# Kernel optimization log

Hardware: AMD Instinct MI355X
Metric: run time of the kernel (lower is better)

Reference implementation:

```python
import jax, jax.numpy as jnp
import numpy as np

GROUP_SIZE = 128
EPS = 1e-6
# AWQ nibble interleave order within each int32
_AWQ_SHIFTS = jnp.array([0, 4, 1, 5, 2, 6, 3, 7], dtype=jnp.uint32) * 4


def dequant_awq(qw, qz, sc, group_size=GROUP_SIZE):
    # qw: (in, out//8) int32, qz: (in//g, out//8) int32, sc: (in//g, out) float
    in_dim = qw.shape[0]
    w4 = ((qw.astype(jnp.uint32)[:, :, None] >> _AWQ_SHIFTS) & 0xF).astype(sc.dtype)
    z4 = ((qz.astype(jnp.uint32)[:, :, None] >> _AWQ_SHIFTS) & 0xF).astype(sc.dtype)
    w4 = w4.reshape(in_dim, -1)                    # (in, out)
    z4 = z4.reshape(qz.shape[0], -1)               # (in//g, out)
    z = jnp.repeat(z4, group_size, axis=0)         # (in, out)
    s = jnp.repeat(sc, group_size, axis=0)         # (in, out)
    return (w4 - z) * s


def rmsnorm(x, w, eps=EPS):
    return x * w * jax.lax.rsqrt(jnp.mean(x * x, axis=-1, keepdims=True) + eps)


def setup_inputs() -> dict:
    key = jax.random.key(0)
    ks = jax.random.split(key, 16)
    H, I, G = 2048, 8192, GROUP_SIZE
    IMAX = 2**31 - 1
    d = {}
    d['x'] = jax.random.normal(ks[0], (2, 2048, H), dtype=jnp.float32)
    d['ln1_w'] = jnp.ones((H,), jnp.float32)
    d['ln2_w'] = jnp.ones((H,), jnp.float32)
    d['qkv_qw'] = jax.random.randint(ks[1], (H, 3 * H // 8), 0, IMAX, dtype=jnp.int32)
    d['qkv_qz'] = jax.random.randint(ks[2], (H // G, 3 * H // 8), 0, IMAX, dtype=jnp.int32)
    d['qkv_sc'] = jax.random.normal(ks[3], (H // G, 3 * H), dtype=jnp.float32) * 0.02
    d['o_qw'] = jax.random.randint(ks[4], (H, H // 8), 0, IMAX, dtype=jnp.int32)
    d['o_qz'] = jax.random.randint(ks[5], (H // G, H // 8), 0, IMAX, dtype=jnp.int32)
    d['o_sc'] = jax.random.normal(ks[6], (H // G, H), dtype=jnp.float32) * 0.02
    d['gu_qw'] = jax.random.randint(ks[7], (H, 2 * I // 8), 0, IMAX, dtype=jnp.int32)
    d['gu_qz'] = jax.random.randint(ks[8], (H // G, 2 * I // 8), 0, IMAX, dtype=jnp.int32)
    d['gu_sc'] = jax.random.normal(ks[9], (H // G, 2 * I), dtype=jnp.float32) * 0.02
    d['dn_qw'] = jax.random.randint(ks[10], (I, H // 8), 0, IMAX, dtype=jnp.int32)
    d['dn_qz'] = jax.random.randint(ks[11], (I // G, H // 8), 0, IMAX, dtype=jnp.int32)
    d['dn_sc'] = jax.random.normal(ks[12], (I // G, H), dtype=jnp.float32) * 0.02
    return d


def reference(x, ln1_w, ln2_w, qkv_qw, qkv_qz, qkv_sc, o_qw, o_qz, o_sc,
              gu_qw, gu_qz, gu_sc, dn_qw, dn_qz, dn_sc):
    H = x.shape[-1]
    # attention-ish block (mock: qkv proj, take q slice, o proj)
    residual = x
    h = rmsnorm(x, ln1_w)
    qkv = h @ dequant_awq(qkv_qw, qkv_qz, qkv_sc)          # (..., 3H)
    q = qkv[..., :H]
    o = q @ dequant_awq(o_qw, o_qz, o_sc)                  # (..., H)
    x = residual + o
    # SwiGLU MLP
    residual = x
    h = rmsnorm(x, ln2_w)
    gate_up = h @ dequant_awq(gu_qw, gu_qz, gu_sc)         # (..., 2I)
    gate, up = jnp.split(gate_up, 2, axis=-1)
    mlp = (jax.nn.silu(gate) * up) @ dequant_awq(dn_qw, dn_qz, dn_sc)
    return residual + mlp
```

## Files before the change

kernel.cpp:

```cpp
#include <hip/hip_runtime.h>
#include <hip/hip_bf16.h>
#include <stdint.h>

typedef __bf16 bf16x8 __attribute__((ext_vector_type(8)));
typedef __bf16 bf16x2 __attribute__((ext_vector_type(2)));
typedef float  f32x4  __attribute__((ext_vector_type(4)));

template <int V> struct ic { static constexpr int value = V; };

__device__ __forceinline__ void gload_lds16(const void* g, void* l) {
  __builtin_amdgcn_global_load_lds(
      (const __attribute__((address_space(1))) void*)g,
      (__attribute__((address_space(3))) void*)l, 16, 0, 0);
}

__global__ __launch_bounds__(256) void rmsnorm_kernel(
    const float* __restrict__ x, const float* __restrict__ w,
    __bf16* __restrict__ out) {
  constexpr int H = 2048;
  const int row = blockIdx.x;
  const int t = threadIdx.x;
  const float4* xr = (const float4*)(x + (size_t)row * H);
  float4 a = xr[t * 2 + 0];
  float4 b = xr[t * 2 + 1];
  float ss = a.x*a.x + a.y*a.y + a.z*a.z + a.w*a.w
           + b.x*b.x + b.y*b.y + b.z*b.z + b.w*b.w;
#pragma unroll
  for (int o = 32; o > 0; o >>= 1) ss += __shfl_xor(ss, o);
  __shared__ float red[4];
  if ((t & 63) == 0) red[t >> 6] = ss;
  __syncthreads();
  float tot = red[0] + red[1] + red[2] + red[3];
  float r = rsqrtf(tot * (1.0f / H) + 1e-6f);
  const float4* wr4 = (const float4*)w;
  float4 wa = wr4[t * 2 + 0];
  float4 wb = wr4[t * 2 + 1];
  bf16x8 ov;
  ov[0] = (__bf16)(a.x * wa.x * r);
  ov[1] = (__bf16)(a.y * wa.y * r);
  ov[2] = (__bf16)(a.z * wa.z * r);
  ov[3] = (__bf16)(a.w * wa.w * r);
  ov[4] = (__bf16)(b.x * wb.x * r);
  ov[5] = (__bf16)(b.y * wb.y * r);
  ov[6] = (__bf16)(b.z * wb.z * r);
  ov[7] = (__bf16)(b.w * wb.w * r);
  *(bf16x8*)(out + (size_t)row * H + (size_t)t * 8) = ov;
}

template <int GU>
__global__ __launch_bounds__(256) void dequant_t_kernel(
    const int* __restrict__ qw, const int* __restrict__ qz,
    const float* __restrict__ sc, __bf16* __restrict__ wt,
    int K, int Cp, int Nfull) {
  const int t = threadIdx.x;
  const int k0 = blockIdx.x * 128 + (t & 63) * 2;
  const int c0 = blockIdx.y * 64 + (t >> 6) * 16;
  const int g = k0 >> 7;
  const uint32_t* qw0 = (const uint32_t*)qw + (size_t)k0 * Cp + c0;
  const uint32_t* qw1 = qw0 + Cp;
  const uint32_t* qzr = (const uint32_t*)qz + (size_t)g * Cp + c0;
  const float* scr = sc + (size_t)g * Nfull + (size_t)c0 * 8;

  uint32_t u0[16], u1[16], z[16];
#pragma unroll
  for (int j = 0; j < 4; j++) {
    *(int4*)(&u0[j*4]) = *(const int4*)(qw0 + j*4);
    *(int4*)(&u1[j*4]) = *(const int4*)(qw1 + j*4);
    *(int4*)(&z[j*4])  = *(const int4*)(qzr + j*4);
  }

#pragma unroll
  for (int i = 0; i < 16; i++) {
#pragma unroll
    for (int s = 0; s < 8; s++) {
      const int sh = ((s >> 1) * 4) + ((s & 1) ? 16 : 0);
      const float zf = (float)((z[i] >> sh) & 15u);
      const float scv = scr[i * 8 + s];
      const float w0 = ((float)((u0[i] >> sh) & 15u) - zf) * scv;
      const float w1 = ((float)((u1[i] >> sh) & 15u) - zf) * scv;
      const int n = (c0 + i) * 8 + s;
      int row;
      if (GU) row = (n < 8192) ? ((n >> 4) * 32 + (n & 15))
                               : (((n - 8192) >> 4) * 32 + 16 + (n & 15));
      else    row = n;
      bf16x2 pv = {(__bf16)w0, (__bf16)w1};
      *(bf16x2*)(wt + (size_t)row * K + k0) = pv;
    }
  }
}

template <int BN, int EPI, int KC>
__global__ __launch_bounds__(512, 2) void gemm8p_kernel(
    const __bf16* __restrict__ A, const __bf16* __restrict__ Bt,
    void* __restrict__ Cv, const float* __restrict__ addend,
    int M, int N) {
  constexpr int NT = KC / 64;
  constexpr int BQ = BN / 64;
  constexpr int NSTRIP = BN / 4;
  constexpr int NI = NSTRIP / 16;

  __shared__ alignas(16) __bf16 As[8 * 4096];
  __shared__ alignas(16) __bf16 Bs[2 * BQ * 4096];

  const int t = threadIdx.x;
  const int w = t >> 6, l = t & 63;
  const int lm = l & 15, kb = l >> 4;
  const int l7 = lm & 7;
  const int wm = w >> 2, wn = w & 3;

  const size_t stat = (size_t)(t >> 3) * KC + (size_t)(((t & 7) ^ ((t >> 3) & 7)) << 3);

  const int nwg = gridDim.x;
  const int bid = blockIdx.x;
  const int swz = (bid & 7) * (nwg >> 3) + (bid >> 3);
  const int nbm = M >> 8;
  const int per_g = nbm * 8;
  const int grp = swz / per_g, v = swz % per_g;
  const int bm0 = (v % nbm) * 256;
  const int bn0 = (grp * 8 + v / nbm) * BN;

  const __bf16* Ab = A + (size_t)bm0 * KC;
  const __bf16* Bb = Bt + (size_t)bn0 * KC;

  const uint32_t gsw0 = (uint32_t)((kb ^ l7) << 4);
  const uint32_t gsw1 = (uint32_t)(((4 + kb) ^ l7) << 4);
  const uint32_t arow = (uint32_t)(wm * 16384 + lm * 128);
  const uint32_t aoff0 = arow + gsw0, aoff1 = arow + gsw1;
  const uint32_t brow = (BN == 256)
      ? (uint32_t)(wn * 8192 + lm * 128)
      : (uint32_t)((wn >> 1) * 8192 + (wn & 1) * 4096 + lm * 128);
  const uint32_t boff0 = brow + gsw0, boff1 = brow + gsw1;
  const char* AsC = (const char*)As;
  const char* BsC = (const char*)Bs;

  f32x4 acc[8][NI] = {};
  bf16x8 af[2][2][2];
  bf16x8 bfr[2][NI][2];

  auto ldAf = [&](int dD, int mi, bf16x8* dst) {
    const uint32_t imA = (uint32_t)((dD * 4 + (mi >> 2)) * 8192 + (mi & 3) * 2048);
    dst[0] = *(const bf16x8*)(AsC + aoff0 + imA);
    dst[1] = *(const bf16x8*)(AsC + aoff1 + imA);
  };
  auto ldBf = [&](int dD) {
#pragma unroll
    for (int ni = 0; ni < NI; ++ni) {
      const uint32_t imB = (uint32_t)(dD * BQ * 8192 + ni * 2048);
      bfr[dD][ni][0] = *(const bf16x8*)(BsC + boff0 + imB);
      bfr[dD][ni][1] = *(const bf16x8*)(BsC + boff1 + imB);
    }
  };
  auto mfma4 = [&](int q, bf16x8 afq[2][2], int dD) {
    __builtin_amdgcn_s_setprio(1);
#pragma unroll
    for (int kk = 0; kk < 2; ++kk)
#pragma unroll
      for (int ni = 0; ni < NI; ++ni)
#pragma unroll
        for (int m2 = 0; m2 < 2; ++m2)
          acc[q * 2 + m2][ni] = __builtin_amdgcn_mfma_f32_16x16x32_bf16(
              afq[m2][kk], bfr[dD][ni][kk], acc[q * 2 + m2][ni], 0, 0, 0);
    __builtin_amdgcn_s_setprio(0);
  };

#pragma unroll
  for (int qa = 0; qa < 4; ++qa)
    gload_lds16(Ab + stat + (size_t)(qa * 64) * KC, As + qa * 4096 + t * 8);
#pragma unroll
  for (int qb = 0; qb < BQ; ++qb)
    gload_lds16(Bb + stat + (size_t)(qb * 64) * KC, Bs + qb * 4096 + t * 8);
#pragma unroll
  for (int qb = 0; qb < BQ; ++qb)
    gload_lds16(Bb + stat + (size_t)(qb * 64) * KC + 64, Bs + (BQ + qb) * 4096 + t * 8);
  gload_lds16(Ab + stat + 64, As + 4 * 4096 + t * 8);
  gload_lds16(Ab + stat + (size_t)128 * KC + 64, As + 6 * 4096 + t * 8);
  if (BN == 256) asm volatile("s_waitcnt vmcnt(6)" ::: "memory");
  else           asm volatile("s_waitcnt vmcnt(4)" ::: "memory");
  __builtin_amdgcn_s_barrier();

  ldAf(0, 0, af[0][0]); ldAf(0, 1, af[0][1]);
  ldBf(0);
  asm volatile("" ::: "memory");

  const __bf16* pA0 = Ab + stat + 128;
  const __bf16* pA1 = Ab + stat + (size_t)64 * KC + 64;
  const __bf16* pA2 = Ab + stat + (size_t)128 * KC + 128;
  const __bf16* pA3 = Ab + stat + (size_t)192 * KC + 64;
  const __bf16* pB0 = Bb + stat + 128;
  const __bf16* pB1 = Bb + stat + (size_t)64 * KC + 128;
  const __bf16* pB2 = Bb + stat + (size_t)128 * KC + 128;
  const __bf16* pB3 = Bb + stat + (size_t)192 * KC + 128;

  auto tile = [&](auto Dc, auto Sc) {
    constexpr int D = decltype(Dc)::value;
    constexpr int STG = decltype(Sc)::value;
    ldAf(D, 2, af[1][0]); ldAf(D, 3, af[1][1]);
    asm volatile("" ::: "memory");
    if (STG >= 1) {
      gload_lds16(pA1, As + ((D ^ 1) * 4 + 1) * 4096 + t * 8);
      gload_lds16(pA3, As + ((D ^ 1) * 4 + 3) * 4096 + t * 8);
    }
    __builtin_amdgcn_s_barrier();
    mfma4(0, af[0], D);
    __builtin_amdgcn_s_barrier();
    ldAf(D, 4, af[0][0]); ldAf(D, 5, af[0][1]);
    asm volatile("" ::: "memory");
    if (STG == 2) {
      gload_lds16(pB0, Bs + (D * BQ + 0) * 4096 + t * 8);
      gload_lds16(pB1, Bs + (D * BQ + 1) * 4096 + t * 8);
    }
    __builtin_amdgcn_s_barrier();
    mfma4(1, af[1], D);
    __builtin_amdgcn_s_barrier();
    ldAf(D, 6, af[1][0]); ldAf(D, 7, af[1][1]);
    asm volatile("" ::: "memory");
    if (STG == 2) {
      if (BN == 256) {
        gload_lds16(pB2, Bs + (D * BQ + 2) * 4096 + t * 8);
        gload_lds16(pB3, Bs + (D * BQ + 3) * 4096 + t * 8);
      } else {
        gload_lds16(pA0, As + (D * 4 + 0) * 4096 + t * 8);
        gload_lds16(pA2, As + (D * 4 + 2) * 4096 + t * 8);
      }
    }
    __builtin_amdgcn_s_barrier();
    mfma4(2, af[0], D);
    __builtin_amdgcn_s_barrier();
    asm volatile("s_waitcnt lgkmcnt(0)" ::: "memory");
    __builtin_amdgcn_sched_barrier(0);
    if (STG == 2)      asm volatile("s_waitcnt vmcnt(4)" ::: "memory");
    else if (STG == 1) asm volatile("s_waitcnt vmcnt(0)" ::: "memory");
    __builtin_amdgcn_s_barrier();
    if (STG >= 1) {
      ldAf(D ^ 1, 0, af[0][0]); ldAf(D ^ 1, 1, af[0][1]);
      ldBf(D ^ 1);
    }
    if (STG == 2 && BN == 256) {
      gload_lds16(pA0, As + (D * 4 + 0) * 4096 + t * 8);
      gload_lds16(pA2, As + (D * 4 + 2) * 4096 + t * 8);
    }
    __builtin_amdgcn_sched_barrier(0);
    mfma4(3, af[1], D);
    __builtin_amdgcn_s_barrier();
    if (STG == 2) {
      pA0 += 64; pA1 += 64; pA2 += 64; pA3 += 64;
      pB0 += 64; pB1 += 64;
      if (BN == 256) { pB2 += 64; pB3 += 64; }
    }
  };

#pragma unroll 1
  for (int it = 0; it < NT / 2 - 1; ++it) {
    tile(ic<0>{}, ic<2>{});
    tile(ic<1>{}, ic<2>{});
  }
  tile(ic<0>{}, ic<1>{});
  tile(ic<1>{}, ic<0>{});

  const int crow0 = bm0 + wm * 128;
#pragma unroll
  for (int mi = 0; mi < 8; ++mi) {
    if (EPI == 2) {
#pragma unroll
      for (int p = 0; p < NI / 2; ++p) {
        const int ni = p * 2;
        const int col = ((bn0 + wn * 64 + ni * 16) >> 5) * 16 + lm;
#pragma unroll
        for (int r = 0; r < 4; ++r) {
          const int row = crow0 + mi * 16 + kb * 4 + r;
          const float gv = acc[mi][ni][r], uv = acc[mi][ni + 1][r];
          const float av = uv * (gv / (1.0f + __expf(-gv)));
          ((__bf16*)Cv)[(size_t)row * 8192 + col] = (__bf16)av;
        }
      }
    } else {
#pragma unroll
      for (int ni = 0; ni < NI; ++ni) {
        const int col = bn0 + wn * NSTRIP + ni * 16 + lm;
#pragma unroll
        for (int r = 0; r < 4; ++r) {
          const int row = crow0 + mi * 16 + kb * 4 + r;
          const size_t idx = (size_t)row * N + col;
          if (EPI == 0) ((__bf16*)Cv)[idx] = (__bf16)acc[mi][ni][r];
          else          ((float*)Cv)[idx] = addend[idx] + acc[mi][ni][r];
        }
      }
    }
  }
}

template <int EPI, int KC>
__global__ __launch_bounds__(512, 4) void gemm128_kernel(
    const __bf16* __restrict__ A, const __bf16* __restrict__ Bt,
    void* __restrict__ Cv, const float* __restrict__ addend,
    int M, int N) {
  constexpr int NT = KC / 64;

  __shared__ alignas(16) __bf16 As[4 * 4096];
  __shared__ alignas(16) __bf16 Bs[4 * 4096];

  const int t = threadIdx.x;
  const int w = t >> 6, l = t & 63;
  const int lm = l & 15, kb = l >> 4;
  const int l7 = lm & 7;
  const int wm = w >> 2, wn = w & 3;

  const size_t stat = (size_t)(t >> 3) * KC + (size_t)(((t & 7) ^ ((t >> 3) & 7)) << 3);

  const int nwg = gridDim.x;
  const int bid = blockIdx.x;
  const int swz = (bid & 7) * (nwg >> 3) + (bid >> 3);
  const int nbm = M >> 7;
  const int per_g = nbm * 8;
  const int grp = swz / per_g, v = swz % per_g;
  const int bm0 = (v % nbm) * 128;
  const int bn0 = (grp * 8 + v / nbm) * 128;

  const __bf16* Ab = A + (size_t)bm0 * KC;
  const __bf16* Bb = Bt + (size_t)bn0 * KC;

  const uint32_t gsw0 = (uint32_t)((kb ^ l7) << 4);
  const uint32_t gsw1 = (uint32_t)(((4 + kb) ^ l7) << 4);
  const uint32_t aoff0 = (uint32_t)((wm * 32 + lm) * 128) + gsw0;
  const uint32_t aoff1 = (uint32_t)((wm * 32 + lm) * 128) + gsw1;
  const uint32_t bbase = (uint32_t)(((wn & 1) * 32 + lm) * 128 + (wn >> 1) * 8192);
  const uint32_t boff0 = bbase + gsw0, boff1 = bbase + gsw1;
  const char* AsC = (const char*)As;
  const char* BsC = (const char*)Bs;

  f32x4 acc[4][2] = {};
  bf16x8 af[2][2];
  bf16x8 bfr[2][2][2];

  auto ldAf = [&](int dD, int mi) {
    const uint32_t imA = (uint32_t)((dD * 2 + (mi >> 1)) * 8192 + (mi & 1) * 2048);
    af[mi & 1][0] = *(const bf16x8*)(AsC + aoff0 + imA);
    af[mi & 1][1] = *(const bf16x8*)(AsC + aoff1 + imA);
  };
  auto ldBf = [&](int dD) {
#pragma unroll
    for (int ni = 0; ni < 2; ++ni) {
      const uint32_t imB = (uint32_t)(dD * 16384 + ni * 2048);
      bfr[dD][ni][0] = *(const bf16x8*)(BsC + boff0 + imB);
      bfr[dD][ni][1] = *(const bf16x8*)(BsC + boff1 + imB);
    }
  };
  auto mfma1 = [&](int mi, int dD) {
    __builtin_amdgcn_s_setprio(1);
#pragma unroll
    for (int kk = 0; kk < 2; ++kk)
#pragma unroll
      for (int ni = 0; ni < 2; ++ni)
        acc[mi][ni] = __builtin_amdgcn_mfma_f32_16x16x32_bf16(
            af[mi & 1][kk], bfr[dD][ni][kk], acc[mi][ni], 0, 0, 0);
    __builtin_amdgcn_s_setprio(0);
  };

  gload_lds16(Ab + stat,                        As + 0 * 4096 + t * 8);
  gload_lds16(Ab + stat + (size_t)64 * KC,      As + 1 * 4096 + t * 8);
  gload_lds16(Bb + stat,                        Bs + 0 * 4096 + t * 8);
  gload_lds16(Bb + stat + (size_t)64 * KC,      Bs + 1 * 4096 + t * 8);
  gload_lds16(Bb + stat + 64,                   Bs + 2 * 4096 + t * 8);
  gload_lds16(Bb + stat + (size_t)64 * KC + 64, Bs + 3 * 4096 + t * 8);
  gload_lds16(Ab + stat + 64,                   As + 2 * 4096 + t * 8);
  asm volatile("s_waitcnt vmcnt(3)" ::: "memory");
  __builtin_amdgcn_s_barrier();

  ldAf(0, 0);
  ldBf(0);
  asm volatile("" ::: "memory");

  const __bf16* pAq1 = Ab + stat + (size_t)64 * KC + 64;
  const __bf16* pAq0 = Ab + stat + 128;
  const __bf16* pBq0 = Bb + stat + 128;
  const __bf16* pBq1 = Bb + stat + (size_t)64 * KC + 128;

  auto tile = [&](auto Dc, auto Sc) {
    constexpr int D = decltype(Dc)::value;
    constexpr int STG = decltype(Sc)::value;
    ldAf(D, 1);
    asm volatile("" ::: "memory");
    if (STG >= 1)
      gload_lds16(pAq1, As + ((D ^ 1) * 2 + 1) * 4096 + t * 8);
    __builtin_amdgcn_s_barrier();
    mfma1(0, D);
    __builtin_amdgcn_s_barrier();
    ldAf(D, 2);
    asm volatile("" ::: "memory");
    if (STG == 2) {
      gload_lds16(pBq0, Bs + (D * 2 + 0) * 4096 + t * 8);
      gload_lds16(pBq1, Bs + (D * 2 + 1) * 4096 + t * 8);
    }
    __builtin_amdgcn_s_barrier();
    mfma1(1, D);
    __builtin_amdgcn_s_barrier();
    ldAf(D, 3);
    asm volatile("" ::: "memory");
    if (STG == 2)
      gload_lds16(pAq0, As + (D * 2 + 0) * 4096 + t * 8);
    __builtin_amdgcn_s_barrier();
    mfma1(2, D);
    __builtin_amdgcn_s_barrier();
    asm volatile("s_waitcnt lgkmcnt(0)" ::: "memory");
    __builtin_amdgcn_sched_barrier(0);
    if (STG == 2)      asm volatile("s_waitcnt vmcnt(3)" ::: "memory");
    else if (STG == 1) asm volatile("s_waitcnt vmcnt(0)" ::: "memory");
    __builtin_amdgcn_s_barrier();
    if (STG >= 1) {
      ldAf(D ^ 1, 0);
      ldBf(D ^ 1);
    }
    __builtin_amdgcn_sched_barrier(0);
    mfma1(3, D);
    __builtin_amdgcn_s_barrier();
    if (STG == 2) { pAq0 += 64; pAq1 += 64; pBq0 += 64; pBq1 += 64; }
  };

#pragma unroll 1
  for (int it = 0; it < NT / 2 - 1; ++it) {
    tile(ic<0>{}, ic<2>{});
    tile(ic<1>{}, ic<2>{});
  }
  tile(ic<0>{}, ic<1>{});
  tile(ic<1>{}, ic<0>{});

#pragma unroll
  for (int mi = 0; mi < 4; ++mi) {
#pragma unroll
    for (int ni = 0; ni < 2; ++ni) {
      const int col = bn0 + wn * 32 + ni * 16 + lm;
#pragma unroll
      for (int r = 0; r < 4; ++r) {
        const int row = bm0 + (mi >> 1) * 64 + wm * 32 + (mi & 1) * 16 + kb * 4 + r;
        const size_t idx = (size_t)row * N + col;
        if (EPI == 0) ((__bf16*)Cv)[idx] = (__bf16)acc[mi][ni][r];
        else          ((float*)Cv)[idx] = addend[idx] + acc[mi][ni][r];
      }
    }
  }
}

extern "C" void kernel_launch(void* const* d_in, const int* in_sizes, int n_in,
                              void* d_out, int out_size, void* d_ws, size_t ws_size,
                              hipStream_t stream) {
  const float* x      = (const float*)d_in[0];
  const float* ln1    = (const float*)d_in[1];
  const float* ln2    = (const float*)d_in[2];
  const int*   qkv_qw = (const int*)d_in[3];
  const int*   qkv_qz = (const int*)d_in[4];
  const float* qkv_sc = (const float*)d_in[5];
  const int*   o_qw   = (const int*)d_in[6];
  const int*   o_qz   = (const int*)d_in[7];
  const float* o_sc   = (const float*)d_in[8];
  const int*   gu_qw  = (const int*)d_in[9];
  const int*   gu_qz  = (const int*)d_in[10];
  const float* gu_sc  = (const float*)d_in[11];
  const int*   dn_qw  = (const int*)d_in[12];
  const int*   dn_qz  = (const int*)d_in[13];
  const float* dn_sc  = (const float*)d_in[14];

  constexpr int M = 4096;

  char* ws = (char*)d_ws;
  __bf16* h   = (__bf16*)(ws + 0);
  __bf16* q   = (__bf16*)(ws + 16777216ULL);
  float*  x2  = (float*)(ws + 33554432ULL);
  __bf16* W   = (__bf16*)(ws + 67108864ULL);
  __bf16* act = (__bf16*)(ws + 134217728ULL);
  __bf16* Wdn = (__bf16*)(ws + 0);

  rmsnorm_kernel<<<dim3(M), dim3(256), 0, stream>>>(x, ln1, h);
  dequant_t_kernel<0><<<dim3(16, 4), dim3(256), 0, stream>>>(qkv_qw, qkv_qz, qkv_sc, W, 2048, 768, 6144);
  gemm128_kernel<0, 2048><<<dim3(512), dim3(512), 0, stream>>>(h, W, (void*)q, nullptr, M, 2048);
  dequant_t_kernel<0><<<dim3(16, 4), dim3(256), 0, stream>>>(o_qw, o_qz, o_sc, W, 2048, 256, 2048);
  gemm128_kernel<1, 2048><<<dim3(512), dim3(512), 0, stream>>>(q, W, (void*)x2, x, M, 2048);
  rmsnorm_kernel<<<dim3(M), dim3(256), 0, stream>>>(x2, ln2, h);
  dequant_t_kernel<1><<<dim3(16, 32), dim3(256), 0, stream>>>(gu_qw, gu_qz, gu_sc, W, 2048, 2048, 16384);
  gemm8p_kernel<256, 2, 2048><<<dim3(1024), dim3(512), 0, stream>>>(h, W, (void*)act, nullptr, M, 16384);
  dequant_t_kernel<0><<<dim3(64, 4), dim3(256), 0, stream>>>(dn_qw, dn_qz, dn_sc, Wdn, 8192, 256, 2048);
  gemm128_kernel<1, 8192><<<dim3(512), dim3(512), 0, stream>>>(act, Wdn, d_out, x2, M, 2048);
}
```

Before: 516.1 us.

## Restructure GEMM inner tiles into quadrant MFMA blocks with in-tile fragment loads

The big gate/up GEMM is specialised to a 256-wide tile, and its inner loop changes from four row-strip MFMA phases into four quadrant phases (4x2 MFMA blocks). Each phase loads its A half and B pair from LDS inside the same tile, which removes the cross-tile prefetch of fragments for the next buffer. The 128 GEMM gets the same quadrant restructure. This cuts register pressure and simplifies the waits. The cost is that LDS fragment loads are no longer hidden behind the previous tile's MFMAs, so phases may stall on LDS latency.

After: 542.3 us. 5.1% more time.

```diff
diff --git a/kernel.cpp b/kernel.cpp
--- a/kernel.cpp
+++ b/kernel.cpp
@@ -89,18 +89,14 @@
   }
 }
 
-template <int BN, int EPI, int KC>
-__global__ __launch_bounds__(512, 2) void gemm8p_kernel(
+template <int KC>
+__global__ __launch_bounds__(512, 2) void gemm256_kernel(
     const __bf16* __restrict__ A, const __bf16* __restrict__ Bt,
-    void* __restrict__ Cv, const float* __restrict__ addend,
-    int M, int N) {
+    __bf16* __restrict__ act, int M) {
   constexpr int NT = KC / 64;
-  constexpr int BQ = BN / 64;
-  constexpr int NSTRIP = BN / 4;
-  constexpr int NI = NSTRIP / 16;
 
   __shared__ alignas(16) __bf16 As[8 * 4096];
-  __shared__ alignas(16) __bf16 Bs[2 * BQ * 4096];
+  __shared__ alignas(16) __bf16 Bs[8 * 4096];
 
   const int t = threadIdx.x;
   const int w = t >> 6, l = t & 63;
@@ -117,7 +113,7 @@
   const int per_g = nbm * 8;
   const int grp = swz / per_g, v = swz % per_g;
   const int bm0 = (v % nbm) * 256;
-  const int bn0 = (grp * 8 + v / nbm) * BN;
+  const int bn0 = (grp * 8 + v / nbm) * 256;
 
   const __bf16* Ab = A + (size_t)bm0 * KC;
   const __bf16* Bb = Bt + (size_t)bn0 * KC;
@@ -126,40 +122,43 @@
   const uint32_t gsw1 = (uint32_t)(((4 + kb) ^ l7) << 4);
   const uint32_t arow = (uint32_t)(wm * 16384 + lm * 128);
   const uint32_t aoff0 = arow + gsw0, aoff1 = arow + gsw1;
-  const uint32_t brow = (BN == 256)
-      ? (uint32_t)(wn * 8192 + lm * 128)
-      : (uint32_t)((wn >> 1) * 8192 + (wn & 1) * 4096 + lm * 128);
+  const uint32_t brow = (uint32_t)(wn * 8192 + lm * 128);
   const uint32_t boff0 = brow + gsw0, boff1 = brow + gsw1;
   const char* AsC = (const char*)As;
   const char* BsC = (const char*)Bs;
 
-  f32x4 acc[8][NI] = {};
-  bf16x8 af[2][2][2];
-  bf16x8 bfr[2][NI][2];
-
-  auto ldAf = [&](int dD, int mi, bf16x8* dst) {
-    const uint32_t imA = (uint32_t)((dD * 4 + (mi >> 2)) * 8192 + (mi & 3) * 2048);
-    dst[0] = *(const bf16x8*)(AsC + aoff0 + imA);
-    dst[1] = *(const bf16x8*)(AsC + aoff1 + imA);
-  };
-  auto ldBf = [&](int dD) {
-#pragma unroll
-    for (int ni = 0; ni < NI; ++ni) {
-      const uint32_t imB = (uint32_t)(dD * BQ * 8192 + ni * 2048);
-      bfr[dD][ni][0] = *(const bf16x8*)(BsC + boff0 + imB);
-      bfr[dD][ni][1] = *(const bf16x8*)(BsC + boff1 + imB);
-    }
-  };
-  auto mfma4 = [&](int q, bf16x8 afq[2][2], int dD) {
+  f32x4 acc[8][4] = {};
+  bf16x8 af4[4][2];
+  bf16x8 bfr4[4][2];
+
+  auto ldAhalf = [&](int dD, int half) {
+#pragma unroll
+    for (int m2 = 0; m2 < 4; ++m2) {
+      const int mi = half * 4 + m2;
+      const uint32_t imA = (uint32_t)((dD * 4 + (mi >> 2)) * 8192 + (mi & 3) * 2048);
+      af4[m2][0] = *(const bf16x8*)(AsC + aoff0 + imA);
+      af4[m2][1] = *(const bf16x8*)(AsC + aoff1 + imA);
+    }
+  };
+  auto ldBpair = [&](int dD, int p) {
+#pragma unroll
+    for (int j = 0; j < 2; ++j) {
+      const int ni = p * 2 + j;
+      const uint32_t imB = (uint32_t)(dD * 32768 + ni * 2048);
+      bfr4[ni][0] = *(const bf16x8*)(BsC + boff0 + imB);
+      bfr4[ni][1] = *(const bf16x8*)(BsC + boff1 + imB);
+    }
+  };
+  auto mfmaQ = [&](int qm, int qn) {
     __builtin_amdgcn_s_setprio(1);
 #pragma unroll
     for (int kk = 0; kk < 2; ++kk)
 #pragma unroll
-      for (int ni = 0; ni < NI; ++ni)
-#pragma unroll
-        for (int m2 = 0; m2 < 2; ++m2)
-          acc[q * 2 + m2][ni] = __builtin_amdgcn_mfma_f32_16x16x32_bf16(
-              afq[m2][kk], bfr[dD][ni][kk], acc[q * 2 + m2][ni], 0, 0, 0);
+      for (int j = 0; j < 2; ++j)
+#pragma unroll
+        for (int m2 = 0; m2 < 4; ++m2)
+          acc[qm * 4 + m2][qn * 2 + j] = __builtin_amdgcn_mfma_f32_16x16x32_bf16(
+              af4[m2][kk], bfr4[qn * 2 + j][kk], acc[qm * 4 + m2][qn * 2 + j], 0, 0, 0);
     __builtin_amdgcn_s_setprio(0);
   };
 
@@ -167,20 +166,15 @@
   for (int qa = 0; qa < 4; ++qa)
     gload_lds16(Ab + stat + (size_t)(qa * 64) * KC, As + qa * 4096 + t * 8);
 #pragma unroll
-  for (int qb = 0; qb < BQ; ++qb)
+  for (int qb = 0; qb < 4; ++qb)
     gload_lds16(Bb + stat + (size_t)(qb * 64) * KC, Bs + qb * 4096 + t * 8);
 #pragma unroll
-  for (int qb = 0; qb < BQ; ++qb)
-    gload_lds16(Bb + stat + (size_t)(qb * 64) * KC + 64, Bs + (BQ + qb) * 4096 + t * 8);
+  for (int qb = 0; qb < 4; ++qb)
+    gload_lds16(Bb + stat + (size_t)(qb * 64) * KC + 64, Bs + (4 + qb) * 4096 + t * 8);
   gload_lds16(Ab + stat + 64, As + 4 * 4096 + t * 8);
   gload_lds16(Ab + stat + (size_t)128 * KC + 64, As + 6 * 4096 + t * 8);
-  if (BN == 256) asm volatile("s_waitcnt vmcnt(6)" ::: "memory");
-  else           asm volatile("s_waitcnt vmcnt(4)" ::: "memory");
+  asm volatile("s_waitcnt vmcnt(6)" ::: "memory");
   __builtin_amdgcn_s_barrier();
-
-  ldAf(0, 0, af[0][0]); ldAf(0, 1, af[0][1]);
-  ldBf(0);
-  asm volatile("" ::: "memory");
 
   const __bf16* pA0 = Ab + stat + 128;
   const __bf16* pA1 = Ab + stat + (size_t)64 * KC + 64;
@@ -194,58 +188,46 @@
   auto tile = [&](auto Dc, auto Sc) {
     constexpr int D = decltype(Dc)::value;
     constexpr int STG = decltype(Sc)::value;
-    ldAf(D, 2, af[1][0]); ldAf(D, 3, af[1][1]);
+    ldAhalf(D, 0);
+    ldBpair(D, 0);
     asm volatile("" ::: "memory");
     if (STG >= 1) {
       gload_lds16(pA1, As + ((D ^ 1) * 4 + 1) * 4096 + t * 8);
       gload_lds16(pA3, As + ((D ^ 1) * 4 + 3) * 4096 + t * 8);
     }
     __builtin_amdgcn_s_barrier();
-    mfma4(0, af[0], D);
-    __builtin_amdgcn_s_barrier();
-    ldAf(D, 4, af[0][0]); ldAf(D, 5, af[0][1]);
+    mfmaQ(0, 0);
+    __builtin_amdgcn_s_barrier();
+    ldBpair(D, 1);
+    asm volatile("" ::: "memory");
+    __builtin_amdgcn_s_barrier();
+    mfmaQ(0, 1);
+    __builtin_amdgcn_s_barrier();
+    ldAhalf(D, 1);
     asm volatile("" ::: "memory");
     if (STG == 2) {
-      gload_lds16(pB0, Bs + (D * BQ + 0) * 4096 + t * 8);
-      gload_lds16(pB1, Bs + (D * BQ + 1) * 4096 + t * 8);
-    }
-    __builtin_amdgcn_s_barrier();
-    mfma4(1, af[1], D);
-    __builtin_amdgcn_s_barrier();
-    ldAf(D, 6, af[1][0]); ldAf(D, 7, af[1][1]);
-    asm volatile("" ::: "memory");
+      gload_lds16(pB0, Bs + (D * 4 + 0) * 4096 + t * 8);
+      gload_lds16(pB1, Bs + (D * 4 + 1) * 4096 + t * 8);
+    }
+    __builtin_amdgcn_s_barrier();
+    mfmaQ(1, 0);
+    __builtin_amdgcn_s_barrier();
+    if (STG == 2)      asm volatile("s_waitcnt vmcnt(2)" ::: "memory");
+    else if (STG == 1) asm volatile("s_waitcnt vmcnt(0)" ::: "memory");
+    __builtin_amdgcn_sched_barrier(0);
+    __builtin_amdgcn_s_barrier();
     if (STG == 2) {
-      if (BN == 256) {
-        gload_lds16(pB2, Bs + (D * BQ + 2) * 4096 + t * 8);
-        gload_lds16(pB3, Bs + (D * BQ + 3) * 4096 + t * 8);
-      } else {
-        gload_lds16(pA0, As + (D * 4 + 0) * 4096 + t * 8);
-        gload_lds16(pA2, As + (D * 4 + 2) * 4096 + t * 8);
-      }
-    }
-    __builtin_amdgcn_s_barrier();
-    mfma4(2, af[0], D);
-    __builtin_amdgcn_s_barrier();
-    asm volatile("s_waitcnt lgkmcnt(0)" ::: "memory");
-    __builtin_amdgcn_sched_barrier(0);
-    if (STG == 2)      asm volatile("s_waitcnt vmcnt(4)" ::: "memory");
-    else if (STG == 1) asm volatile("s_waitcnt vmcnt(0)" ::: "memory");
-    __builtin_amdgcn_s_barrier();
-    if (STG >= 1) {
-      ldAf(D ^ 1, 0, af[0][0]); ldAf(D ^ 1, 1, af[0][1]);
-      ldBf(D ^ 1);
-    }
-    if (STG == 2 && BN == 256) {
+      gload_lds16(pB2, Bs + (D * 4 + 2) * 4096 + t * 8);
+      gload_lds16(pB3, Bs + (D * 4 + 3) * 4096 + t * 8);
       gload_lds16(pA0, As + (D * 4 + 0) * 4096 + t * 8);
       gload_lds16(pA2, As + (D * 4 + 2) * 4096 + t * 8);
     }
     __builtin_amdgcn_sched_barrier(0);
-    mfma4(3, af[1], D);
+    mfmaQ(1, 1);
     __builtin_amdgcn_s_barrier();
     if (STG == 2) {
       pA0 += 64; pA1 += 64; pA2 += 64; pA3 += 64;
-      pB0 += 64; pB1 += 64;
-      if (BN == 256) { pB2 += 64; pB3 += 64; }
+      pB0 += 64; pB1 += 64; pB2 += 64; pB3 += 64;
     }
   };
 
@@ -260,30 +242,16 @@
   const int crow0 = bm0 + wm * 128;
 #pragma unroll
   for (int mi = 0; mi < 8; ++mi) {
-    if (EPI == 2) {
-#pragma unroll
-      for (int p = 0; p < NI / 2; ++p) {
-        const int ni = p * 2;
-        const int col = ((bn0 + wn * 64 + ni * 16) >> 5) * 16 + lm;
-#pragma unroll
-        for (int r = 0; r < 4; ++r) {
-          const int row = crow0 + mi * 16 + kb * 4 + r;
-          const float gv = acc[mi][ni][r], uv = acc[mi][ni + 1][r];
-          const float av = uv * (gv / (1.0f + __expf(-gv)));
-          ((__bf16*)Cv)[(size_t)row * 8192 + col] = (__bf16)av;
-        }
-      }
-    } else {
-#pragma unroll
-      for (int ni = 0; ni < NI; ++ni) {
-        const int col = bn0 + wn * NSTRIP + ni * 16 + lm;
-#pragma unroll
-        for (int r = 0; r < 4; ++r) {
-          const int row = crow0 + mi * 16 + kb * 4 + r;
-          const size_t idx = (size_t)row * N + col;
-          if (EPI == 0) ((__bf16*)Cv)[idx] = (__bf16)acc[mi][ni][r];
-          else          ((float*)Cv)[idx] = addend[idx] + acc[mi][ni][r];
-        }
+#pragma unroll
+    for (int p = 0; p < 2; ++p) {
+      const int ni = p * 2;
+      const int col = ((bn0 + wn * 64 + ni * 16) >> 5) * 16 + lm;
+#pragma unroll
+      for (int r = 0; r < 4; ++r) {
+        const int row = crow0 + mi * 16 + kb * 4 + r;
+        const float gv = acc[mi][ni][r], uv = acc[mi][ni + 1][r];
+        const float av = uv * (gv / (1.0f + __expf(-gv)));
+        act[(size_t)row * 8192 + col] = (__bf16)av;
       }
     }
   }
@@ -329,30 +297,31 @@
   const char* BsC = (const char*)Bs;
 
   f32x4 acc[4][2] = {};
-  bf16x8 af[2][2];
-  bf16x8 bfr[2][2][2];
-
-  auto ldAf = [&](int dD, int mi) {
-    const uint32_t imA = (uint32_t)((dD * 2 + (mi >> 1)) * 8192 + (mi & 1) * 2048);
-    af[mi & 1][0] = *(const bf16x8*)(AsC + aoff0 + imA);
-    af[mi & 1][1] = *(const bf16x8*)(AsC + aoff1 + imA);
-  };
-  auto ldBf = [&](int dD) {
-#pragma unroll
-    for (int ni = 0; ni < 2; ++ni) {
-      const uint32_t imB = (uint32_t)(dD * 16384 + ni * 2048);
-      bfr[dD][ni][0] = *(const bf16x8*)(BsC + boff0 + imB);
-      bfr[dD][ni][1] = *(const bf16x8*)(BsC + boff1 + imB);
-    }
-  };
-  auto mfma1 = [&](int mi, int dD) {
+  bf16x8 af2[2][2];
+  bf16x8 bfrq[2][2];
+
+  auto ldApair = [&](int dD, int half) {
+#pragma unroll
+    for (int m2 = 0; m2 < 2; ++m2) {
+      const int mi = half * 2 + m2;
+      const uint32_t imA = (uint32_t)((dD * 2 + (mi >> 1)) * 8192 + (mi & 1) * 2048);
+      af2[m2][0] = *(const bf16x8*)(AsC + aoff0 + imA);
+      af2[m2][1] = *(const bf16x8*)(AsC + aoff1 + imA);
+    }
+  };
+  auto ldBq = [&](int dD, int ni) {
+    const uint32_t imB = (uint32_t)(dD * 16384 + ni * 2048);
+    bfrq[ni][0] = *(const bf16x8*)(BsC + boff0 + imB);
+    bfrq[ni][1] = *(const bf16x8*)(BsC + boff1 + imB);
+  };
+  auto mfmaQ = [&](int qm, int ni) {
     __builtin_amdgcn_s_setprio(1);
 #pragma unroll
     for (int kk = 0; kk < 2; ++kk)
 #pragma unroll
-      for (int ni = 0; ni < 2; ++ni)
-        acc[mi][ni] = __builtin_amdgcn_mfma_f32_16x16x32_bf16(
-            af[mi & 1][kk], bfr[dD][ni][kk], acc[mi][ni], 0, 0, 0);
+      for (int m2 = 0; m2 < 2; ++m2)
+        acc[qm * 2 + m2][ni] = __builtin_amdgcn_mfma_f32_16x16x32_bf16(
+            af2[m2][kk], bfrq[ni][kk], acc[qm * 2 + m2][ni], 0, 0, 0);
     __builtin_amdgcn_s_setprio(0);
   };
 
@@ -366,10 +335,6 @@
   asm volatile("s_waitcnt vmcnt(3)" ::: "memory");
   __builtin_amdgcn_s_barrier();
 
-  ldAf(0, 0);
-  ldBf(0);
-  asm volatile("" ::: "memory");
-
   const __bf16* pAq1 = Ab + stat + (size_t)64 * KC + 64;
   const __bf16* pAq0 = Ab + stat + 128;
   const __bf16* pBq0 = Bb + stat + 128;
@@ -378,40 +343,34 @@
   auto tile = [&](auto Dc, auto Sc) {
     constexpr int D = decltype(Dc)::value;
     constexpr int STG = decltype(Sc)::value;
-    ldAf(D, 1);
+    ldApair(D, 0);
+    ldBq(D, 0);
     asm volatile("" ::: "memory");
     if (STG >= 1)
       gload_lds16(pAq1, As + ((D ^ 1) * 2 + 1) * 4096 + t * 8);
     __builtin_amdgcn_s_barrier();
-    mfma1(0, D);
-    __builtin_amdgcn_s_barrier();
-    ldAf(D, 2);
+    mfmaQ(0, 0);
+    __builtin_amdgcn_s_barrier();
+    ldBq(D, 1);
+    asm volatile("" ::: "memory");
+    __builtin_amdgcn_s_barrier();
+    mfmaQ(0, 1);
+    __builtin_amdgcn_s_barrier();
+    ldApair(D, 1);
     asm volatile("" ::: "memory");
     if (STG == 2) {
       gload_lds16(pBq0, Bs + (D * 2 + 0) * 4096 + t * 8);
       gload_lds16(pBq1, Bs + (D * 2 + 1) * 4096 + t * 8);
-    }
-    __builtin_amdgcn_s_barrier();
-    mfma1(1, D);
-    __builtin_amdgcn_s_barrier();
-    ldAf(D, 3);
-    asm volatile("" ::: "memory");
-    if (STG == 2)
       gload_lds16(pAq0, As + (D * 2 + 0) * 4096 + t * 8);
-    __builtin_amdgcn_s_barrier();
-    mfma1(2, D);
-    __builtin_amdgcn_s_barrier();
-    asm volatile("s_waitcnt lgkmcnt(0)" ::: "memory");
-    __builtin_amdgcn_sched_barrier(0);
+    }
+    __builtin_amdgcn_s_barrier();
+    mfmaQ(1, 0);
+    __builtin_amdgcn_s_barrier();
     if (STG == 2)      asm volatile("s_waitcnt vmcnt(3)" ::: "memory");
     else if (STG == 1) asm volatile("s_waitcnt vmcnt(0)" ::: "memory");
-    __builtin_amdgcn_s_barrier();
-    if (STG >= 1) {
-      ldAf(D ^ 1, 0);
-      ldBf(D ^ 1);
-    }
     __builtin_amdgcn_sched_barrier(0);
-    mfma1(3, D);
+    __builtin_amdgcn_s_barrier();
+    mfmaQ(1, 1);
     __builtin_amdgcn_s_barrier();
     if (STG == 2) { pAq0 += 64; pAq1 += 64; pBq0 += 64; pBq1 += 64; }
   };
@@ -476,7 +435,7 @@
   gemm128_kernel<1, 2048><<<dim3(512), dim3(512), 0, stream>>>(q, W, (void*)x2, x, M, 2048);
   rmsnorm_kernel<<<dim3(M), dim3(256), 0, stream>>>(x2, ln2, h);
   dequant_t_kernel<1><<<dim3(16, 32), dim3(256), 0, stream>>>(gu_qw, gu_qz, gu_sc, W, 2048, 2048, 16384);
-  gemm8p_kernel<256, 2, 2048><<<dim3(1024), dim3(512), 0, stream>>>(h, W, (void*)act, nullptr, M, 16384);
+  gemm256_kernel<2048><<<dim3(1024), dim3(512), 0, stream>>>(h, W, act, M);
   dequant_t_kernel<0><<<dim3(64, 4), dim3(256), 0, stream>>>(dn_qw, dn_qz, dn_sc, Wdn, 8192, 256, 2048);
   gemm128_kernel<1, 8192><<<dim3(512), dim3(512), 0, stream>>>(act, Wdn, d_out, x2, M, 2048);
 }
```
